# Performance work log

Hardware: AMD Instinct MI355X
Metric: run time of the kernel (lower is better)

## Reference

```python
import jax, jax.numpy as jnp
import numpy as np


def setup_inputs() -> dict:
    key = jax.random.key(0)
    k1, k2, k3 = jax.random.split(key, 3)
    n_sup, n_qry, d, n_classes = 512, 2097152, 64, 16
    support_features = jax.random.normal(k1, (n_sup, d), dtype=jnp.float32)
    query_features = jax.random.normal(k2, (n_qry, d), dtype=jnp.float32)
    support_labels = jnp.arange(n_sup, dtype=jnp.int64) % n_classes  # every class populated
    query_labels = jax.random.randint(k3, (n_qry,), 0, n_classes, dtype=jnp.int64)
    return {
        "support_features": support_features,
        "query_features": query_features,
        "support_labels": support_labels,
        "query_labels": query_labels,
        "n_classes": n_classes,
        "n_iter": 50,
        "beta": 5,
    }


def _sq_dists(q, q_sq, centroids):
    # squared Euclidean distances [Nq, C]; q_sq precomputed row norms of q
    return q_sq[:, None] - 2.0 * (q @ centroids.T) + jnp.sum(centroids * centroids, axis=-1)[None, :]


def reference(support_features, query_features, support_labels, query_labels, n_classes, n_iter, beta):
    dtype = support_features.dtype
    beta_f = jnp.asarray(beta, dtype)
    # per-class support sums/counts (hard assignments, fixed across iterations)
    oh = jax.nn.one_hot(support_labels, n_classes, dtype=dtype)        # [Ns, C]
    class_counts = jnp.sum(oh, axis=0)                                  # [C]
    sup_sum = oh.T @ support_features                                   # [C, d]
    centroids = sup_sum / class_counts[:, None]                         # class means init

    q_sq = jnp.sum(query_features * query_features, axis=-1)            # [Nq]

    def step(centroids, _):
        d2 = _sq_dists(query_features, q_sq, centroids)                 # [Nq, C]
        w = jax.nn.softmax(-beta_f * d2, axis=-1)                       # soft assignments
        num = sup_sum + w.T @ query_features                            # [C, d]
        den = class_counts + jnp.sum(w, axis=0)                         # [C]
        return num / den[:, None], None

    centroids, _ = jax.lax.scan(step, centroids, None, length=n_iter)

    d2 = _sq_dists(query_features, q_sq, centroids)
    pred = jnp.argmin(d2, axis=-1)
    acc = jnp.mean((pred == query_labels).astype(jnp.float32))
    return acc
```

## Files before the change

kernel.cpp:

```cpp
#include <hip/hip_runtime.h>
#include <stdint.h>

typedef short bf16x8 __attribute__((ext_vector_type(8)));
typedef float f32x4 __attribute__((ext_vector_type(4)));
typedef float f32x2 __attribute__((ext_vector_type(2)));
typedef uint32_t u32x4 __attribute__((ext_vector_type(4)));
typedef uint32_t u32x2 __attribute__((ext_vector_type(2)));
typedef unsigned short u16;
typedef long long i64;

#define ITERS 50
#define BETA_F 5.0f

#define WS_SUPSUM 0
#define WS_COUNTS 1024
#define WS_CENT   1040
#define WS_CSQ    2064
#define WS_ACC    2080
#define WS_CORR   10400
#define WS_Q8_OFF 10432

__device__ __forceinline__ u16 f2bf(float x) {
  union { float f; uint32_t u; } v; v.f = x;
  uint32_t r = (v.u + 0x7FFFu + ((v.u >> 16) & 1u)) >> 16;
  return (u16)r;
}
__device__ __forceinline__ float bf2f(u16 b) {
  union { float f; uint32_t u; } v; v.u = ((uint32_t)b) << 16;
  return v.f;
}
__device__ __forceinline__ float u2f(uint32_t u) {
  union { float f; uint32_t u; } v; v.u = u;
  return v.f;
}
__device__ __forceinline__ uint32_t fkey(float f) {
  union { float f; uint32_t u; } v; v.f = f;
  return (v.u & 0x80000000u) ? ~v.u : (v.u | 0x80000000u);
}
__device__ __forceinline__ uint32_t cvt_pk_bf16(float a, float b) {
  uint32_t r;
  asm("v_cvt_pk_bf16_f32 %0, %1, %2" : "=v"(r) : "v"(a), "v"(b));
  return r;
}
__device__ __forceinline__ uint32_t pk8(float a, float b, float c, float d) {
  int r = __builtin_amdgcn_cvt_pk_fp8_f32(a, b, 0, false);
  r = __builtin_amdgcn_cvt_pk_fp8_f32(c, d, r, true);
  return (uint32_t)r;
}
__device__ __forceinline__ i64 pack64(uint32_t lo, uint32_t hi) {
  return (i64)(((uint64_t)hi << 32) | (uint64_t)lo);
}
__device__ __forceinline__ void quant_hilo4(float v0, float v1, float v2, float v3,
                                            uint32_t& hi, uint32_t& lo, float& sq) {
  uint32_t h = pk8(v0, v1, v2, v3);
  float h0 = __builtin_amdgcn_cvt_f32_fp8((int)h, 0);
  float h1 = __builtin_amdgcn_cvt_f32_fp8((int)h, 1);
  float h2 = __builtin_amdgcn_cvt_f32_fp8((int)h, 2);
  float h3 = __builtin_amdgcn_cvt_f32_fp8((int)h, 3);
  uint32_t l = pk8(v0 - h0, v1 - h1, v2 - h2, v3 - h3);
  float c0 = h0 + __builtin_amdgcn_cvt_f32_fp8((int)l, 0);
  float c1 = h1 + __builtin_amdgcn_cvt_f32_fp8((int)l, 1);
  float c2 = h2 + __builtin_amdgcn_cvt_f32_fp8((int)l, 2);
  float c3 = h3 + __builtin_amdgcn_cvt_f32_fp8((int)l, 3);
  sq += c0 * c0 + c1 * c1 + c2 * c2 + c3 * c3;
  hi = h; lo = l;
}

template <int CTRL>
__device__ __forceinline__ float dppf(float x) {
  int i = __builtin_bit_cast(int, x);
  int r = __builtin_amdgcn_update_dpp(i, i, CTRL, 0xF, 0xF, false);
  return __builtin_bit_cast(float, r);
}
template <int CTRL>
__device__ __forceinline__ uint32_t dppu(uint32_t x) {
  int r = __builtin_amdgcn_update_dpp((int)x, (int)x, CTRL, 0xF, 0xF, false);
  return (uint32_t)r;
}
__device__ __forceinline__ float rmax16(float x) {
  x = fmaxf(x, dppf<0xB1>(x));
  x = fmaxf(x, dppf<0x4E>(x));
  x = fmaxf(x, dppf<0x141>(x));
  x = fmaxf(x, dppf<0x140>(x));
  return x;
}
__device__ __forceinline__ float rsum16(float x) {
  x += dppf<0xB1>(x);
  x += dppf<0x4E>(x);
  x += dppf<0x141>(x);
  x += dppf<0x140>(x);
  return x;
}
__device__ __forceinline__ uint32_t rumax16(uint32_t x) {
  uint32_t t;
  t = dppu<0xB1>(x);  x = (t > x) ? t : x;
  t = dppu<0x4E>(x);  x = (t > x) ? t : x;
  t = dppu<0x141>(x); x = (t > x) ? t : x;
  t = dppu<0x140>(x); x = (t > x) ? t : x;
  return x;
}

__global__ __launch_bounds__(1024) void init_kernel(const float* __restrict__ sup,
                                                    const int* __restrict__ slab,
                                                    int NS, float* __restrict__ ws) {
  const int tid = threadIdx.x;
  const int c = tid >> 6, j = tid & 63;
  float s = 0.f; int cnt = 0;
  for (int i = 0; i < NS; ++i) {
    int lbl = slab[i];
    float v = sup[i * 64 + j];
    if (lbl == c) { s += v; cnt++; }
  }
  ws[WS_SUPSUM + tid] = s;
  if (j == 0) ws[WS_COUNTS + c] = (float)cnt;
  ws[WS_CENT + tid] = s / (float)cnt;
  for (int i = tid; i < 8 * 1040; i += 1024) ws[WS_ACC + i] = 0.f;
  if (tid == 0) ws[WS_CORR] = 0.f;
  __syncthreads();
  if (j == 0) {
    float sq = 0.f;
    for (int k = 0; k < 64; ++k) { float v = ws[WS_CENT + c * 64 + k]; sq += v * v; }
    ws[WS_CSQ + c] = sq;
  }
}

__global__ __launch_bounds__(256) void convert_kernel(const float* __restrict__ qf,
                                                      u32x4* __restrict__ q8, int n16) {
  const int start = blockIdx.x * 256 + threadIdx.x;
  const int stride = gridDim.x * 256;
  const f32x4* in = (const f32x4*)qf;
  for (int k = start; k < n16; k += stride) {
    f32x4 v0 = in[4 * k + 0], v1 = in[4 * k + 1], v2 = in[4 * k + 2], v3 = in[4 * k + 3];
    u32x4 o;
    o[0] = pk8(v0[0], v0[1], v0[2], v0[3]);
    o[1] = pk8(v1[0], v1[1], v1[2], v1[3]);
    o[2] = pk8(v2[0], v2[1], v2[2], v2[3]);
    o[3] = pk8(v3[0], v3[1], v3[2], v3[3]);
    q8[k] = o;
  }
}

template <bool SRC_F8>
__global__ __launch_bounds__(256, 4) void pass_kernel(const float* __restrict__ qf,
                                                      const uint8_t* __restrict__ q8,
                                                      int NQ, float* __restrict__ ws) {
  __shared__ __attribute__((aligned(16))) uint32_t qt_w[4][64][16];
  __shared__ __attribute__((aligned(16))) u16 w_lds[4][16][32];
  __shared__ float redden[16];

  const int tid = threadIdx.x;
  const int lane = tid & 63;
  const int wv = tid >> 6;
  const int c = lane & 15;
  const int g = lane >> 4;

  const float* cent = ws + WS_CENT;
  const int cb = c * 64 + g * 8;
  uint32_t bh0a, bl0a, bh0b, bl0b, bh1a, bl1a, bh1b, bl1b;
  float csq = 0.f;
  quant_hilo4(cent[cb + 0], cent[cb + 1], cent[cb + 2], cent[cb + 3], bh0a, bl0a, csq);
  quant_hilo4(cent[cb + 4], cent[cb + 5], cent[cb + 6], cent[cb + 7], bh0b, bl0b, csq);
  quant_hilo4(cent[cb + 32], cent[cb + 33], cent[cb + 34], cent[cb + 35], bh1a, bl1a, csq);
  quant_hilo4(cent[cb + 36], cent[cb + 37], cent[cb + 38], cent[cb + 39], bh1b, bl1b, csq);
  csq += __shfl_xor(csq, 16);
  csq += __shfl_xor(csq, 32);
  const i64 bh0 = pack64(bh0a, bh0b), bl0 = pack64(bl0a, bl0b);
  const i64 bh1 = pack64(bh1a, bh1b), bl1 = pack64(bl1a, bl1b);

  f32x4 acc[4];
#pragma unroll
  for (int nt = 0; nt < 4; ++nt) acc[nt] = (f32x4){0.f, 0.f, 0.f, 0.f};
  float denacc = 0.f;

  const uint32_t psel = (c & 1) ? 0x03020706u : 0x05040100u;

  const int wave_id = blockIdx.x * 4 + wv;
  const int nwaves = gridDim.x * 4;
  const int ntiles = NQ >> 5;

  for (int tile = wave_id; tile < ntiles; tile += nwaves) {
    const int qbase = tile << 5;
#pragma unroll
    for (int st = 0; st < 2; ++st) {
      const int q = qbase + st * 16 + c;
      u32x2 a0u, a1u;
      if (SRC_F8) {
        const uint8_t* qrow = q8 + (size_t)q * 64;
        a0u = *(const u32x2*)(qrow + g * 8);
        a1u = *(const u32x2*)(qrow + 32 + g * 8);
      } else {
        const float* qrow = qf + (size_t)q * 64 + g * 8;
        a0u[0] = pk8(qrow[0], qrow[1], qrow[2], qrow[3]);
        a0u[1] = pk8(qrow[4], qrow[5], qrow[6], qrow[7]);
        a1u[0] = pk8(qrow[32], qrow[33], qrow[34], qrow[35]);
        a1u[1] = pk8(qrow[36], qrow[37], qrow[38], qrow[39]);
      }
      const i64 a0 = __builtin_bit_cast(i64, a0u);
      const i64 a1 = __builtin_bit_cast(i64, a1u);
      f32x4 sc = (f32x4){0.f, 0.f, 0.f, 0.f};
      sc = __builtin_amdgcn_mfma_f32_16x16x32_fp8_fp8(a0, bh0, sc, 0, 0, 0);
      sc = __builtin_amdgcn_mfma_f32_16x16x32_fp8_fp8(a0, bl0, sc, 0, 0, 0);
      sc = __builtin_amdgcn_mfma_f32_16x16x32_fp8_fp8(a1, bh1, sc, 0, 0, 0);
      sc = __builtin_amdgcn_mfma_f32_16x16x32_fp8_fp8(a1, bl1, sc, 0, 0, 0);
      float wr[4];
#pragma unroll
      for (int r = 0; r < 4; ++r) {
        float sv = BETA_F * (2.f * sc[r] - csq);
        float m = rmax16(sv);
        float e = __expf(sv - m);
        float s = rsum16(e);
        wr[r] = e * __builtin_amdgcn_rcpf(s);
      }
      uint32_t wlo = cvt_pk_bf16(wr[0], wr[1]);
      uint32_t whi = cvt_pk_bf16(wr[2], wr[3]);
      *(uint2*)&w_lds[wv][c][st * 16 + g * 4] = make_uint2(wlo, whi);
      denacc += u2f(wlo << 16) + u2f(wlo & 0xFFFF0000u) +
                u2f(whi << 16) + u2f(whi & 0xFFFF0000u);

      uint32_t ua[4], ub[4];
      {
        f32x2 t0 = __builtin_amdgcn_cvt_pk_f32_fp8((int)a0u[0], false);
        f32x2 t1 = __builtin_amdgcn_cvt_pk_f32_fp8((int)a0u[0], true);
        f32x2 t2 = __builtin_amdgcn_cvt_pk_f32_fp8((int)a0u[1], false);
        f32x2 t3 = __builtin_amdgcn_cvt_pk_f32_fp8((int)a0u[1], true);
        ua[0] = cvt_pk_bf16(t0[0], t0[1]);
        ua[1] = cvt_pk_bf16(t1[0], t1[1]);
        ua[2] = cvt_pk_bf16(t2[0], t2[1]);
        ua[3] = cvt_pk_bf16(t3[0], t3[1]);
        t0 = __builtin_amdgcn_cvt_pk_f32_fp8((int)a1u[0], false);
        t1 = __builtin_amdgcn_cvt_pk_f32_fp8((int)a1u[0], true);
        t2 = __builtin_amdgcn_cvt_pk_f32_fp8((int)a1u[1], false);
        t3 = __builtin_amdgcn_cvt_pk_f32_fp8((int)a1u[1], true);
        ub[0] = cvt_pk_bf16(t0[0], t0[1]);
        ub[1] = cvt_pk_bf16(t1[0], t1[1]);
        ub[2] = cvt_pk_bf16(t2[0], t2[1]);
        ub[3] = cvt_pk_bf16(t3[0], t3[1]);
      }
      const int drow = g * 8 + (c & 1);
      const int wcol = ((st << 3) + (c >> 1)) ^ (g << 2);
#pragma unroll
      for (int p = 0; p < 4; ++p) {
        uint32_t m0 = ua[p];
        uint32_t n0 = dppu<0xB1>(m0);
        qt_w[wv][drow + 2 * p][wcol] = __builtin_amdgcn_perm(n0, m0, psel);
        uint32_t m1 = ub[p];
        uint32_t n1 = dppu<0xB1>(m1);
        qt_w[wv][32 + drow + 2 * p][wcol] = __builtin_amdgcn_perm(n1, m1, psel);
      }
    }
    bf16x8 aw = *(const bf16x8*)&w_lds[wv][c][g * 8];
#pragma unroll
    for (int nt = 0; nt < 4; ++nt) {
      const int K = ((nt << 1) + (c >> 3)) & 3;
      bf16x8 bq = *(const bf16x8*)&qt_w[wv][nt * 16 + c][(g ^ K) << 2];
      acc[nt] = __builtin_amdgcn_mfma_f32_16x16x32_bf16(aw, bq, acc[nt], 0, 0, 0);
    }
  }

  __syncthreads();
  float* red = (float*)&qt_w[0][0][0];
  for (int i = tid; i < 1024; i += 256) red[i] = 0.f;
  if (tid < 16) redden[tid] = 0.f;
  __syncthreads();
#pragma unroll
  for (int nt = 0; nt < 4; ++nt)
#pragma unroll
    for (int r = 0; r < 4; ++r)
      atomicAdd(&red[(g * 4 + r) * 64 + nt * 16 + c], acc[nt][r]);
  atomicAdd(&redden[c], denacc);
  __syncthreads();
  float* accn = ws + WS_ACC + (size_t)(blockIdx.x & 7) * 1040;
  for (int i = tid; i < 1024; i += 256) atomicAdd(&accn[i], red[i]);
  if (tid < 16) atomicAdd(&accn[1024 + tid], redden[tid]);
}

__global__ __launch_bounds__(1024) void update_kernel(float* __restrict__ ws) {
  const int tid = threadIdx.x;
  const int c = tid >> 6;
  float num = ws[WS_SUPSUM + tid];
  float den = ws[WS_COUNTS + c];
#pragma unroll
  for (int rep = 0; rep < 8; ++rep) {
    num += ws[WS_ACC + rep * 1040 + tid];
    den += ws[WS_ACC + rep * 1040 + 1024 + c];
  }
  ws[WS_CENT + tid] = num / den;
  for (int i = tid; i < 8 * 1040; i += 1024) ws[WS_ACC + i] = 0.f;
  __syncthreads();
  if ((tid & 63) == 0) {
    float sq = 0.f;
    for (int k = 0; k < 64; ++k) { float v = ws[WS_CENT + c * 64 + k]; sq += v * v; }
    ws[WS_CSQ + c] = sq;
  }
}

__global__ __launch_bounds__(256, 4) void final_kernel(const float* __restrict__ qf,
                                                       const int* __restrict__ qlab,
                                                       int NQ, float* __restrict__ ws) {
  const int tid = threadIdx.x;
  const int lane = tid & 63;
  const int c = lane & 15;
  const int g = lane >> 4;

  const float* cent = ws + WS_CENT;
  bf16x8 bc0, bc1;
#pragma unroll
  for (int j = 0; j < 8; ++j) {
    bc0[j] = (short)f2bf(cent[c * 64 + g * 8 + j]);
    bc1[j] = (short)f2bf(cent[c * 64 + 32 + g * 8 + j]);
  }
  const float csq = ws[WS_CSQ + c];

  int cnt = 0;
  const int wave_id = blockIdx.x * 4 + (tid >> 6);
  const int nwaves = gridDim.x * 4;
  const int ntiles = NQ >> 4;

  for (int tile = wave_id; tile < ntiles; tile += nwaves) {
    const int qbase = tile << 4;
    const int q = qbase + c;
    const float* qrow = qf + (size_t)q * 64;
    bf16x8 a0, a1;
#pragma unroll
    for (int j = 0; j < 8; ++j) {
      a0[j] = (short)f2bf(qrow[g * 8 + j]);
      a1[j] = (short)f2bf(qrow[32 + g * 8 + j]);
    }
    f32x4 sc = (f32x4){0.f, 0.f, 0.f, 0.f};
    sc = __builtin_amdgcn_mfma_f32_16x16x32_bf16(a0, bc0, sc, 0, 0, 0);
    sc = __builtin_amdgcn_mfma_f32_16x16x32_bf16(a1, bc1, sc, 0, 0, 0);
#pragma unroll
    for (int r = 0; r < 4; ++r) {
      float val = 2.f * sc[r] - csq;
      uint32_t key = (fkey(val) & 0xFFFFFFF0u) | (uint32_t)(15 - c);
      key = rumax16(key);
      int pred = 15 - (int)(key & 15u);
      if (c == 0) cnt += (qlab[qbase + g * 4 + r] == pred) ? 1 : 0;
    }
  }
#pragma unroll
  for (int msk = 1; msk < 64; msk <<= 1) cnt += __shfl_xor(cnt, msk);
  if (lane == 0) atomicAdd(&ws[WS_CORR], (float)cnt);
}

__global__ void finalize_kernel(const float* __restrict__ ws, float* __restrict__ out, float inv) {
  out[0] = ws[WS_CORR] * inv;
}

extern "C" void kernel_launch(void* const* d_in, const int* in_sizes, int n_in,
                              void* d_out, int out_size, void* d_ws, size_t ws_size,
                              hipStream_t stream) {
  const float* sup = (const float*)d_in[0];
  const float* qf  = (const float*)d_in[1];
  const int* slab  = (const int*)d_in[2];
  const int* qlab  = (const int*)d_in[3];
  float* ws = (float*)d_ws;
  float* out = (float*)d_out;
  const int NS = in_sizes[0] / 64;
  const int NQ = in_sizes[1] / 64;
  uint8_t* q8 = (uint8_t*)(ws + WS_Q8_OFF);
  const size_t need = (size_t)WS_Q8_OFF * 4 + (size_t)NQ * 64;
  const bool use_f8 = (ws_size >= need);

  init_kernel<<<1, 1024, 0, stream>>>(sup, slab, NS, ws);
  if (use_f8) convert_kernel<<<4096, 256, 0, stream>>>(qf, (u32x4*)q8, NQ * 4);
  for (int it = 0; it < ITERS; ++it) {
    if (use_f8) pass_kernel<true><<<2048, 256, 0, stream>>>(qf, q8, NQ, ws);
    else        pass_kernel<false><<<2048, 256, 0, stream>>>(qf, q8, NQ, ws);
    update_kernel<<<1, 1024, 0, stream>>>(ws);
  }
  final_kernel<<<2048, 256, 0, stream>>>(qf, qlab, NQ, ws);
  finalize_kernel<<<1, 1, 0, stream>>>(ws, out, 1.0f / (float)NQ);
}
```

Measured before the change: 5.881 ms.

## Use fp8 second GEMM with LDS transpose-read, fuse conversion, prefetch next tile

The w^T·Q accumulation GEMM switches from bf16 to fp8: soft weights are packed to fp8, and the query tile is stored as fp8 bytes in LDS and read back transposed with ds_read_b64_tr_b8. This removes the per-tile fp8→bf16 conversion and DPP/perm shuffle work. The separate convert kernel is dropped; the first pass converts fp32 queries to fp8 and writes them out, and the next tile's queries are software-prefetched into registers. It also uses a single 16-byte load per row in place of two 8-byte loads. The cost is lower precision in the weights and the numerator accumulation, plus reliance on the transpose-read instruction.

```diff
diff --git a/kernel.cpp b/kernel.cpp
--- a/kernel.cpp
+++ b/kernel.cpp
@@ -6,6 +6,7 @@
 typedef float f32x2 __attribute__((ext_vector_type(2)));
 typedef uint32_t u32x4 __attribute__((ext_vector_type(4)));
 typedef uint32_t u32x2 __attribute__((ext_vector_type(2)));
+typedef int i32x2 __attribute__((ext_vector_type(2)));
 typedef unsigned short u16;
 typedef long long i64;
 
@@ -25,22 +26,9 @@
   uint32_t r = (v.u + 0x7FFFu + ((v.u >> 16) & 1u)) >> 16;
   return (u16)r;
 }
-__device__ __forceinline__ float bf2f(u16 b) {
-  union { float f; uint32_t u; } v; v.u = ((uint32_t)b) << 16;
-  return v.f;
-}
-__device__ __forceinline__ float u2f(uint32_t u) {
-  union { float f; uint32_t u; } v; v.u = u;
-  return v.f;
-}
 __device__ __forceinline__ uint32_t fkey(float f) {
   union { float f; uint32_t u; } v; v.f = f;
   return (v.u & 0x80000000u) ? ~v.u : (v.u | 0x80000000u);
-}
-__device__ __forceinline__ uint32_t cvt_pk_bf16(float a, float b) {
-  uint32_t r;
-  asm("v_cvt_pk_bf16_f32 %0, %1, %2" : "=v"(r) : "v"(a), "v"(b));
-  return r;
 }
 __device__ __forceinline__ uint32_t pk8(float a, float b, float c, float d) {
   int r = __builtin_amdgcn_cvt_pk_fp8_f32(a, b, 0, false);
@@ -66,6 +54,25 @@
   hi = h; lo = l;
 }
 
+__device__ __forceinline__ i32x2 ds_tr8(const uint8_t* p) {
+#if defined(__has_builtin)
+#if __has_builtin(__builtin_amdgcn_ds_read_tr8_b64)
+#define HAVE_TR8 1
+#endif
+#endif
+#ifdef HAVE_TR8
+  typedef __attribute__((address_space(3))) i32x2 lds_i32x2;
+  return __builtin_amdgcn_ds_read_tr8_b64((lds_i32x2*)p);
+#else
+  uint32_t off = (uint32_t)(uintptr_t)(__attribute__((address_space(3))) const void*)p;
+  i32x2 r;
+  asm volatile("ds_read_b64_tr_b8 %0, %1\n\ts_waitcnt lgkmcnt(0)"
+               : "=v"(r) : "v"(off) : "memory");
+  __builtin_amdgcn_sched_barrier(0);
+  return r;
+#endif
+}
+
 template <int CTRL>
 __device__ __forceinline__ float dppf(float x) {
   int i = __builtin_bit_cast(int, x);
@@ -124,28 +131,12 @@
   }
 }
 
-__global__ __launch_bounds__(256) void convert_kernel(const float* __restrict__ qf,
-                                                      u32x4* __restrict__ q8, int n16) {
-  const int start = blockIdx.x * 256 + threadIdx.x;
-  const int stride = gridDim.x * 256;
-  const f32x4* in = (const f32x4*)qf;
-  for (int k = start; k < n16; k += stride) {
-    f32x4 v0 = in[4 * k + 0], v1 = in[4 * k + 1], v2 = in[4 * k + 2], v3 = in[4 * k + 3];
-    u32x4 o;
-    o[0] = pk8(v0[0], v0[1], v0[2], v0[3]);
-    o[1] = pk8(v1[0], v1[1], v1[2], v1[3]);
-    o[2] = pk8(v2[0], v2[1], v2[2], v2[3]);
-    o[3] = pk8(v3[0], v3[1], v3[2], v3[3]);
-    q8[k] = o;
-  }
-}
-
-template <bool SRC_F8>
+template <bool SRC_F8, bool WRC8>
 __global__ __launch_bounds__(256, 4) void pass_kernel(const float* __restrict__ qf,
-                                                      const uint8_t* __restrict__ q8,
+                                                      uint8_t* __restrict__ q8,
                                                       int NQ, float* __restrict__ ws) {
-  __shared__ __attribute__((aligned(16))) uint32_t qt_w[4][64][16];
-  __shared__ __attribute__((aligned(16))) u16 w_lds[4][16][32];
+  __shared__ __attribute__((aligned(16))) uint8_t qt8[4][2048];
+  __shared__ __attribute__((aligned(16))) uint8_t w8[4][16][32];
   __shared__ float redden[16];
 
   const int tid = threadIdx.x;
@@ -166,99 +157,92 @@
   csq += __shfl_xor(csq, 32);
   const i64 bh0 = pack64(bh0a, bh0b), bl0 = pack64(bl0a, bl0b);
   const i64 bh1 = pack64(bh1a, bh1b), bl1 = pack64(bl1a, bl1b);
-
-  f32x4 acc[4];
-#pragma unroll
-  for (int nt = 0; nt < 4; ++nt) acc[nt] = (f32x4){0.f, 0.f, 0.f, 0.f};
+  const float kcn = -BETA_F * csq;
+
+  f32x4 acc[4] = {};
   float denacc = 0.f;
 
-  const uint32_t psel = (c & 1) ? 0x03020706u : 0x05040100u;
+  uint8_t* qtw = &qt8[wv][0];
+  const uint8_t* trb = qtw + c + g * 128;
+  uint8_t* w8w = &w8[wv][c][0];
+  const int woff = (g >> 1) * 512 + (g & 1) * 8;
 
   const int wave_id = blockIdx.x * 4 + wv;
   const int nwaves = gridDim.x * 4;
   const int ntiles = NQ >> 5;
 
-  for (int tile = wave_id; tile < ntiles; tile += nwaves) {
-    const int qbase = tile << 5;
+  auto LOADQ = [&](int tl, u32x2 (&da)[2], u32x2 (&db)[2]) {
+    const int qb0 = tl << 5;
 #pragma unroll
     for (int st = 0; st < 2; ++st) {
-      const int q = qbase + st * 16 + c;
-      u32x2 a0u, a1u;
+      const int q = qb0 + st * 16 + c;
       if (SRC_F8) {
-        const uint8_t* qrow = q8 + (size_t)q * 64;
-        a0u = *(const u32x2*)(qrow + g * 8);
-        a1u = *(const u32x2*)(qrow + 32 + g * 8);
+        u32x4 v = *(const u32x4*)(q8 + (size_t)q * 64 + g * 16);
+        da[st][0] = v[0]; da[st][1] = v[1];
+        db[st][0] = v[2]; db[st][1] = v[3];
       } else {
-        const float* qrow = qf + (size_t)q * 64 + g * 8;
-        a0u[0] = pk8(qrow[0], qrow[1], qrow[2], qrow[3]);
-        a0u[1] = pk8(qrow[4], qrow[5], qrow[6], qrow[7]);
-        a1u[0] = pk8(qrow[32], qrow[33], qrow[34], qrow[35]);
-        a1u[1] = pk8(qrow[36], qrow[37], qrow[38], qrow[39]);
+        const float* qr = qf + (size_t)q * 64 + g * 8;
+        f32x4 v0 = *(const f32x4*)(qr);
+        f32x4 v1 = *(const f32x4*)(qr + 4);
+        f32x4 v2 = *(const f32x4*)(qr + 32);
+        f32x4 v3 = *(const f32x4*)(qr + 36);
+        da[st][0] = pk8(v0[0], v0[1], v0[2], v0[3]);
+        da[st][1] = pk8(v1[0], v1[1], v1[2], v1[3]);
+        db[st][0] = pk8(v2[0], v2[1], v2[2], v2[3]);
+        db[st][1] = pk8(v3[0], v3[1], v3[2], v3[3]);
+        if (WRC8) {
+          u32x4 o; o[0] = da[st][0]; o[1] = da[st][1]; o[2] = db[st][0]; o[3] = db[st][1];
+          *(u32x4*)(q8 + (size_t)q * 64 + g * 16) = o;
+        }
       }
-      const i64 a0 = __builtin_bit_cast(i64, a0u);
-      const i64 a1 = __builtin_bit_cast(i64, a1u);
-      f32x4 sc = (f32x4){0.f, 0.f, 0.f, 0.f};
-      sc = __builtin_amdgcn_mfma_f32_16x16x32_fp8_fp8(a0, bh0, sc, 0, 0, 0);
-      sc = __builtin_amdgcn_mfma_f32_16x16x32_fp8_fp8(a0, bl0, sc, 0, 0, 0);
-      sc = __builtin_amdgcn_mfma_f32_16x16x32_fp8_fp8(a1, bh1, sc, 0, 0, 0);
-      sc = __builtin_amdgcn_mfma_f32_16x16x32_fp8_fp8(a1, bl1, sc, 0, 0, 0);
+    }
+  };
+
+  u32x2 qa[2] = {}, qb_[2] = {}, na_[2] = {}, nb_[2] = {};
+  int tile = wave_id;
+  if (tile < ntiles) LOADQ(tile, qa, qb_);
+  for (; tile < ntiles; tile += nwaves) {
+    if (tile + nwaves < ntiles) LOADQ(tile + nwaves, na_, nb_);
+#pragma unroll
+    for (int st = 0; st < 2; ++st) {
+      const int row = st * 16 + c;
+      *(u32x2*)(qtw + woff + row * 16) = qa[st];
+      *(u32x2*)(qtw + woff + row * 16 + 1024) = qb_[st];
+      const i64 a0 = __builtin_bit_cast(i64, qa[st]);
+      const i64 a1 = __builtin_bit_cast(i64, qb_[st]);
+      f32x4 sc4 = {};
+      sc4 = __builtin_amdgcn_mfma_f32_16x16x32_fp8_fp8(a0, bh0, sc4, 0, 0, 0);
+      sc4 = __builtin_amdgcn_mfma_f32_16x16x32_fp8_fp8(a0, bl0, sc4, 0, 0, 0);
+      sc4 = __builtin_amdgcn_mfma_f32_16x16x32_fp8_fp8(a1, bh1, sc4, 0, 0, 0);
+      sc4 = __builtin_amdgcn_mfma_f32_16x16x32_fp8_fp8(a1, bl1, sc4, 0, 0, 0);
       float wr[4];
 #pragma unroll
       for (int r = 0; r < 4; ++r) {
-        float sv = BETA_F * (2.f * sc[r] - csq);
+        float sv = fmaf(sc4[r], 2.0f * BETA_F, kcn);
         float m = rmax16(sv);
         float e = __expf(sv - m);
         float s = rsum16(e);
         wr[r] = e * __builtin_amdgcn_rcpf(s);
       }
-      uint32_t wlo = cvt_pk_bf16(wr[0], wr[1]);
-      uint32_t whi = cvt_pk_bf16(wr[2], wr[3]);
-      *(uint2*)&w_lds[wv][c][st * 16 + g * 4] = make_uint2(wlo, whi);
-      denacc += u2f(wlo << 16) + u2f(wlo & 0xFFFF0000u) +
-                u2f(whi << 16) + u2f(whi & 0xFFFF0000u);
-
-      uint32_t ua[4], ub[4];
-      {
-        f32x2 t0 = __builtin_amdgcn_cvt_pk_f32_fp8((int)a0u[0], false);
-        f32x2 t1 = __builtin_amdgcn_cvt_pk_f32_fp8((int)a0u[0], true);
-        f32x2 t2 = __builtin_amdgcn_cvt_pk_f32_fp8((int)a0u[1], false);
-        f32x2 t3 = __builtin_amdgcn_cvt_pk_f32_fp8((int)a0u[1], true);
-        ua[0] = cvt_pk_bf16(t0[0], t0[1]);
-        ua[1] = cvt_pk_bf16(t1[0], t1[1]);
-        ua[2] = cvt_pk_bf16(t2[0], t2[1]);
-        ua[3] = cvt_pk_bf16(t3[0], t3[1]);
-        t0 = __builtin_amdgcn_cvt_pk_f32_fp8((int)a1u[0], false);
-        t1 = __builtin_amdgcn_cvt_pk_f32_fp8((int)a1u[0], true);
-        t2 = __builtin_amdgcn_cvt_pk_f32_fp8((int)a1u[1], false);
-        t3 = __builtin_amdgcn_cvt_pk_f32_fp8((int)a1u[1], true);
-        ub[0] = cvt_pk_bf16(t0[0], t0[1]);
-        ub[1] = cvt_pk_bf16(t1[0], t1[1]);
-        ub[2] = cvt_pk_bf16(t2[0], t2[1]);
-        ub[3] = cvt_pk_bf16(t3[0], t3[1]);
-      }
-      const int drow = g * 8 + (c & 1);
-      const int wcol = ((st << 3) + (c >> 1)) ^ (g << 2);
-#pragma unroll
-      for (int p = 0; p < 4; ++p) {
-        uint32_t m0 = ua[p];
-        uint32_t n0 = dppu<0xB1>(m0);
-        qt_w[wv][drow + 2 * p][wcol] = __builtin_amdgcn_perm(n0, m0, psel);
-        uint32_t m1 = ub[p];
-        uint32_t n1 = dppu<0xB1>(m1);
-        qt_w[wv][32 + drow + 2 * p][wcol] = __builtin_amdgcn_perm(n1, m1, psel);
-      }
-    }
-    bf16x8 aw = *(const bf16x8*)&w_lds[wv][c][g * 8];
+      uint32_t w32 = pk8(wr[0], wr[1], wr[2], wr[3]);
+      *(uint32_t*)(w8w + st * 16 + g * 4) = w32;
+      f32x2 d0 = __builtin_amdgcn_cvt_pk_f32_fp8((int)w32, false);
+      f32x2 d1 = __builtin_amdgcn_cvt_pk_f32_fp8((int)w32, true);
+      denacc += (d0[0] + d0[1]) + (d1[0] + d1[1]);
+    }
+    const i64 aw = *(const i64*)(w8w + g * 8);
 #pragma unroll
     for (int nt = 0; nt < 4; ++nt) {
-      const int K = ((nt << 1) + (c >> 3)) & 3;
-      bf16x8 bq = *(const bf16x8*)&qt_w[wv][nt * 16 + c][(g ^ K) << 2];
-      acc[nt] = __builtin_amdgcn_mfma_f32_16x16x32_bf16(aw, bq, acc[nt], 0, 0, 0);
-    }
-  }
-
-  __syncthreads();
-  float* red = (float*)&qt_w[0][0][0];
+      i32x2 bq = ds_tr8(trb + nt * 512);
+      acc[nt] = __builtin_amdgcn_mfma_f32_16x16x32_fp8_fp8(
+          aw, __builtin_bit_cast(i64, bq), acc[nt], 0, 0, 0);
+    }
+#pragma unroll
+    for (int st = 0; st < 2; ++st) { qa[st] = na_[st]; qb_[st] = nb_[st]; }
+  }
+
+  __syncthreads();
+  float* red = (float*)&qt8[0][0];
   for (int i = tid; i < 1024; i += 256) red[i] = 0.f;
   if (tid < 16) redden[tid] = 0.f;
   __syncthreads();
@@ -363,10 +347,14 @@
   const bool use_f8 = (ws_size >= need);
 
   init_kernel<<<1, 1024, 0, stream>>>(sup, slab, NS, ws);
-  if (use_f8) convert_kernel<<<4096, 256, 0, stream>>>(qf, (u32x4*)q8, NQ * 4);
   for (int it = 0; it < ITERS; ++it) {
-    if (use_f8) pass_kernel<true><<<2048, 256, 0, stream>>>(qf, q8, NQ, ws);
-    else        pass_kernel<false><<<2048, 256, 0, stream>>>(qf, q8, NQ, ws);
+    if (it == 0) {
+      if (use_f8) pass_kernel<false, true><<<2048, 256, 0, stream>>>(qf, q8, NQ, ws);
+      else        pass_kernel<false, false><<<2048, 256, 0, stream>>>(qf, q8, NQ, ws);
+    } else {
+      if (use_f8) pass_kernel<true, false><<<2048, 256, 0, stream>>>(qf, q8, NQ, ws);
+      else        pass_kernel<false, false><<<2048, 256, 0, stream>>>(qf, q8, NQ, ws);
+    }
     update_kernel<<<1, 1024, 0, stream>>>(ws);
   }
   final_kernel<<<2048, 256, 0, stream>>>(qf, qlab, NQ, ws);
```

After: 5.244 ms. 1.12x faster.
